# Kernel tuning notes

Hardware: AMD Instinct MI355X
Metric: run time of the kernel (lower is better)

## Reference

```python
import jax, jax.numpy as jnp
import numpy as np

DIM = 1024
HEADS = 8
DIM_HEAD = DIM // HEADS  # 128
INNER = HEADS * DIM_HEAD  # 1024
EPS = 1e-5


def _xavier(key, shape):
    fan_out, fan_in = shape
    limit = float(np.sqrt(6.0 / (fan_in + fan_out)))
    return jax.random.uniform(key, shape, jnp.float32, -limit, limit)


def setup_inputs() -> dict:
    key = jax.random.key(0)
    ks = jax.random.split(key, 5)
    bs, patch = 16, 2048
    q = jax.random.normal(ks[0], (bs, patch, DIM), jnp.float32)
    kv = jax.random.normal(ks[1], (bs, patch, DIM), jnp.float32)
    Wq = _xavier(ks[2], (INNER, DIM))          # torch Linear weight [out, in]
    Wkv = _xavier(ks[3], (2 * INNER, DIM))
    Wo = _xavier(ks[4], (DIM, INNER))
    gamma_m = jnp.ones((DIM,), jnp.float32)
    beta_m = jnp.zeros((DIM,), jnp.float32)
    gamma_l = jnp.ones((DIM,), jnp.float32)
    beta_l = jnp.zeros((DIM,), jnp.float32)
    return {"q": q, "kv": kv, "gamma_m": gamma_m, "beta_m": beta_m,
            "gamma_l": gamma_l, "beta_l": beta_l, "Wq": Wq, "Wkv": Wkv, "Wo": Wo}


def _layernorm(x, gamma, beta):
    mu = jnp.mean(x, axis=-1, keepdims=True)
    var = jnp.mean(jnp.square(x - mu), axis=-1, keepdims=True)
    return (x - mu) * jax.lax.rsqrt(var + EPS) * gamma + beta


def reference(q, kv, gamma_m, beta_m, gamma_l, beta_l, Wq, Wkv, Wo):
    bs, patch, _ = kv.shape
    scale = DIM_HEAD ** (-0.5)
    qn = _layernorm(q, gamma_m, beta_m)
    kvn = _layernorm(kv, gamma_l, beta_l)
    query = qn @ Wq.T                               # [bs, patch, inner]
    kv_proj = kvn @ Wkv.T                           # [bs, patch, 2*inner]
    key_, value = jnp.split(kv_proj, 2, axis=-1)
    query = query.reshape(bs, patch, HEADS, DIM_HEAD)
    key_ = key_.reshape(bs, patch, HEADS, DIM_HEAD)
    value = value.reshape(bs, patch, HEADS, DIM_HEAD)
    # NOTE: faithful to source: heads axis is NOT moved to batch, so
    # attention is over the HEADS dim per position: scores [bs, patch, heads, heads]
    scores = jnp.einsum('bphd,bpgd->bphg', query, key_) * scale
    weights = jax.nn.softmax(scores, axis=-1)
    context = jnp.einsum('bphg,bpgd->bphd', weights, value)
    context = context.reshape(bs, patch, INNER)
    return context @ Wo.T
```

## Files before the change

kernel.cpp:

```cpp
#include <hip/hip_runtime.h>

typedef unsigned short ushort_t;
typedef __attribute__((ext_vector_type(4))) unsigned short ushort4_t;
typedef __attribute__((ext_vector_type(8))) unsigned short ushort8;
typedef __attribute__((ext_vector_type(8))) __bf16 bf16x8;
typedef __attribute__((ext_vector_type(4))) float f32x4;

typedef const unsigned int __attribute__((address_space(1)))* gas_ptr;
typedef unsigned int __attribute__((address_space(3)))* las_ptr;

__device__ __forceinline__ float b2f(unsigned short u) {
    union { unsigned int i; float f; } x; x.i = ((unsigned int)u) << 16; return x.f;
}
__device__ __forceinline__ unsigned short f2b(float f) {
    union { float f; unsigned int i; } x; x.f = f;
    unsigned int r = (x.i + 0x7fffu + ((x.i >> 16) & 1u)) >> 16;
    return (unsigned short)r;
}

__global__ __launch_bounds__(256) void cvt_kernel(const float* __restrict__ wq,
        const float* __restrict__ wkv, const float* __restrict__ wo,
        ushort_t* __restrict__ yq, ushort_t* __restrict__ ykv, ushort_t* __restrict__ yo) {
    int b = blockIdx.x;
    const float* x; ushort_t* y; size_t off;
    if (b < 1024)      { x = wq;  y = yq;  off = (size_t)b * 1024; }
    else if (b < 3072) { x = wkv; y = ykv; off = (size_t)(b - 1024) * 1024; }
    else               { x = wo;  y = yo;  off = (size_t)(b - 3072) * 1024; }
    size_t i = off + threadIdx.x * 4;
    f32x4 v = *(const f32x4*)(x + i);
    ushort4_t o;
    #pragma unroll
    for (int t = 0; t < 4; ++t) o[t] = f2b(v[t]);
    *(ushort4_t*)(y + i) = o;
}

__global__ __launch_bounds__(256) void ln_kernel(const float* __restrict__ x,
        const float* __restrict__ gamma, const float* __restrict__ beta,
        ushort_t* __restrict__ y) {
    int wave = threadIdx.x >> 6, lane = threadIdx.x & 63;
    size_t row = (size_t)blockIdx.x * 4 + wave;
    const float* xr = x + row * 1024;
    f32x4 v[4];
    #pragma unroll
    for (int c = 0; c < 4; ++c) v[c] = *(const f32x4*)(xr + c * 256 + lane * 4);
    float s = 0.f, s2 = 0.f;
    #pragma unroll
    for (int c = 0; c < 4; ++c)
        #pragma unroll
        for (int t = 0; t < 4; ++t) { s += v[c][t]; s2 += v[c][t] * v[c][t]; }
    #pragma unroll
    for (int off = 1; off < 64; off <<= 1) {
        s  += __shfl_xor(s,  off, 64);
        s2 += __shfl_xor(s2, off, 64);
    }
    float mean = s * (1.0f / 1024.0f);
    float var  = fmaxf(s2 * (1.0f / 1024.0f) - mean * mean, 0.f);
    float rstd = rsqrtf(var + 1e-5f);
    ushort_t* yr = y + row * 1024;
    #pragma unroll
    for (int c = 0; c < 4; ++c) {
        f32x4 g = *(const f32x4*)(gamma + c * 256 + lane * 4);
        f32x4 b = *(const f32x4*)(beta  + c * 256 + lane * 4);
        ushort4_t o;
        #pragma unroll
        for (int t = 0; t < 4; ++t)
            o[t] = f2b((v[c][t] - mean) * rstd * g[t] + b[t]);
        *(ushort4_t*)(yr + c * 256 + lane * 4) = o;
    }
}


#define STG_A(BUFB, RBASE, KT) \
    __builtin_amdgcn_global_load_lds((gas_ptr)(Ap + (size_t)(RBASE) * K + (KT)), \
        (las_ptr)(lds + (BUFB) * 32768 + (RBASE) * 64 + tid * 8), 16, 0, 0)
#define STG_B(BUFB, RBASE, KT) \
    __builtin_amdgcn_global_load_lds((gas_ptr)(Bp + (size_t)(RBASE) * K + (KT)), \
        (las_ptr)(lds + (BUFB) * 32768 + 16384 + (RBASE) * 64 + tid * 8), 16, 0, 0)

#define RD_A(CB, QM) do { _Pragma("unroll") \
    for (int fm = 0; fm < 4; ++fm) { \
        a[fm][0] = *(const bf16x8*)(lds + (CB) * 32768 + aB + (QM) * 4096 + fm * 1024 + ce0); \
        a[fm][1] = *(const bf16x8*)(lds + (CB) * 32768 + aB + (QM) * 4096 + fm * 1024 + ce1); \
    } } while (0)
#define RD_B(CB, QN, BV) do { _Pragma("unroll") \
    for (int fn = 0; fn < 2; ++fn) { \
        BV[fn][0] = *(const bf16x8*)(lds + (CB) * 32768 + bB + (QN) * 2048 + fn * 1024 + ce0); \
        BV[fn][1] = *(const bf16x8*)(lds + (CB) * 32768 + bB + (QN) * 2048 + fn * 1024 + ce1); \
    } } while (0)

#define MFMA_Q(QM, QN, BV) do { _Pragma("unroll") \
    for (int fm = 0; fm < 4; ++fm) { _Pragma("unroll") \
        for (int fn = 0; fn < 2; ++fn) { \
            acc[(QM) * 4 + fm][(QN) * 2 + fn] = __builtin_amdgcn_mfma_f32_16x16x32_bf16( \
                a[fm][0], BV[fn][0], acc[(QM) * 4 + fm][(QN) * 2 + fn], 0, 0, 0); \
            acc[(QM) * 4 + fm][(QN) * 2 + fn] = __builtin_amdgcn_mfma_f32_16x16x32_bf16( \
                a[fm][1], BV[fn][1], acc[(QM) * 4 + fm][(QN) * 2 + fn], 0, 0, 0); \
    } } } while (0)

#define PH_PRE() do { __builtin_amdgcn_s_barrier(); \
    asm volatile("s_waitcnt lgkmcnt(0)" ::: "memory"); \
    __builtin_amdgcn_s_setprio(1); } while (0)
#define PH_POST() do { __builtin_amdgcn_s_setprio(0); \
    __builtin_amdgcn_s_barrier(); } while (0)

#define KTILE(CB, KTN, KTNN) do { \
     \
    STG_A((CB) ^ 1, 64, KTN); STG_A((CB) ^ 1, 192, KTN); \
    RD_A(CB, 0); RD_B(CB, 0, b0); \
    PH_PRE(); MFMA_Q(0, 0, b0); PH_POST(); \
     \
    STG_B((CB) ^ 1, 128, KTN); STG_B((CB) ^ 1, 192, KTN); \
    RD_B(CB, 1, b1); \
    PH_PRE(); MFMA_Q(0, 1, b1); PH_POST(); \
     \
    STG_A(CB, 0, KTNN); STG_A(CB, 128, KTNN); \
    RD_A(CB, 1); \
    PH_PRE(); MFMA_Q(1, 0, b0); PH_POST(); \
     \
    STG_B(CB, 0, KTNN); STG_B(CB, 64, KTNN); \
    PH_PRE(); MFMA_Q(1, 1, b1); \
    __builtin_amdgcn_s_setprio(0); \
    asm volatile("s_waitcnt vmcnt(4)" ::: "memory"); \
    __builtin_amdgcn_s_barrier(); \
} while (0)

template <bool OUT_F32>
__global__ __launch_bounds__(512) void gemm256(const ushort_t* __restrict__ A,
        const ushort_t* __restrict__ B, void* __restrict__ Cv,
        int M, int N, int K) {
    __shared__ ushort_t lds[65536];
    const int tid = threadIdx.x;
    const int lane = tid & 63;
    const int wid = tid >> 6;
    const int wr = wid >> 2, wc = wid & 3;
    const int r16 = lane & 15, q4 = lane >> 4;

    const unsigned nwgx = gridDim.x;
    const unsigned lin = blockIdx.y * nwgx + blockIdx.x;
    const unsigned chunk = (nwgx * gridDim.y) >> 3;
    const unsigned nl = (lin & 7) * chunk + (lin >> 3);
    const int m0 = (int)(nl / nwgx) * 256, n0 = (int)(nl % nwgx) * 256;
    const int NT = K >> 6;

    const int rA = tid >> 3;
    const int cS = ((tid & 7) * 8) ^ ((rA & 7) * 8);
    const ushort_t* Ap = A + (size_t)(m0 + rA) * K + cS;
    const ushort_t* Bp = B + (size_t)(n0 + rA) * K + cS;

    const int ce0 = (q4 * 8) ^ ((lane & 7) * 8);
    const int ce1 = ce0 ^ 32;
    const int aB = (wr * 128 + r16) * 64;
    const int bB = 16384 + (wc * 64 + r16) * 64;

    f32x4 acc[8][4];
    #pragma unroll
    for (int i = 0; i < 8; ++i)
        #pragma unroll
        for (int j = 0; j < 4; ++j)
            acc[i][j] = (f32x4){0.f, 0.f, 0.f, 0.f};
    bf16x8 a[4][2], b0[2][2], b1[2][2];

    STG_A(0, 0, 0); STG_A(0, 128, 0); STG_B(0, 0, 0); STG_B(0, 64, 0);
    STG_A(0, 64, 0); STG_A(0, 192, 0); STG_B(0, 128, 0); STG_B(0, 192, 0);
    STG_A(1, 0, 64); STG_A(1, 128, 64); STG_B(1, 0, 64); STG_B(1, 64, 64);
    asm volatile("s_waitcnt vmcnt(4)" ::: "memory");
    __builtin_amdgcn_s_barrier();

    for (int tt = 0; tt < (NT >> 1); ++tt) {
        const int t = tt << 1;
        const int k1 = (t + 1) << 6;
        int k2 = (t + 2) << 6; if (k2 > K - 64) k2 = K - 64;
        int k3 = (t + 3) << 6; if (k3 > K - 64) k3 = K - 64;
        KTILE(0, k1, k2);
        KTILE(1, k2, k3);
    }

    #pragma unroll
    for (int fm = 0; fm < 8; ++fm) {
        #pragma unroll
        for (int rr = 0; rr < 4; ++rr) {
            int rowC = m0 + wr * 128 + fm * 16 + q4 * 4 + rr;
            if (OUT_F32) {
                float* Cr = (float*)Cv + (size_t)rowC * N + n0 + wc * 64 + r16;
                #pragma unroll
                for (int fn = 0; fn < 4; ++fn)
                    Cr[fn * 16] = acc[fm][fn][rr];
            } else {
                ushort_t* Cr = (ushort_t*)Cv + (size_t)rowC * N + n0 + wc * 64 + r16;
                #pragma unroll
                for (int fn = 0; fn < 4; ++fn)
                    Cr[fn * 16] = f2b(acc[fm][fn][rr]);
            }
        }
    }
}

__global__ __launch_bounds__(256) void attn_kernel(const ushort_t* qin,
        const ushort_t* kvin, ushort_t* outp) {
    __shared__ ushort_t sm[4 * 3072];
    int wave = threadIdx.x >> 6, lane = threadIdx.x & 63;
    size_t p = (size_t)blockIdx.x * 4 + wave;
    ushort_t* sQ = sm + wave * 3072;
    ushort_t* sKV = sQ + 1024;
    const ushort_t* qp  = qin  + p * 1024;
    const ushort_t* kvp = kvin + p * 2048;
    *(ushort8*)(sQ + lane * 8)       = *(const ushort8*)(qp + lane * 8);
    *(ushort8*)(sQ + 512 + lane * 8) = *(const ushort8*)(qp + 512 + lane * 8);
    #pragma unroll
    for (int s = 0; s < 4; ++s)
        *(ushort8*)(sKV + s * 512 + lane * 8) = *(const ushort8*)(kvp + s * 512 + lane * 8);
    __syncthreads();
    int h = lane >> 3;
    int g = lane & 7;
    float sc = 0.f;
    #pragma unroll
    for (int j = 0; j < 128; j += 8) {
        ushort8 a = *(const ushort8*)(sQ + h * 128 + j);
        ushort8 k = *(const ushort8*)(sKV + g * 128 + j);
        #pragma unroll
        for (int t = 0; t < 8; ++t) sc += b2f(a[t]) * b2f(k[t]);
    }
    sc *= 0.08838834764831845f;
    float mx = sc;
    mx = fmaxf(mx, __shfl_xor(mx, 1, 64));
    mx = fmaxf(mx, __shfl_xor(mx, 2, 64));
    mx = fmaxf(mx, __shfl_xor(mx, 4, 64));
    float e = __expf(sc - mx);
    float den = e;
    den += __shfl_xor(den, 1, 64);
    den += __shfl_xor(den, 2, 64);
    den += __shfl_xor(den, 4, 64);
    float w = e / den;
    int d0 = (lane & 7) * 16;
    int gb = lane & 56;
    float accv[16];
    #pragma unroll
    for (int t = 0; t < 16; ++t) accv[t] = 0.f;
    #pragma unroll
    for (int gg = 0; gg < 8; ++gg) {
        float wg = __shfl(w, gb + gg, 64);
        const ushort_t* vr = sKV + 1024 + gg * 128 + d0;
        ushort8 x0 = *(const ushort8*)(vr);
        ushort8 x1 = *(const ushort8*)(vr + 8);
        #pragma unroll
        for (int t = 0; t < 8; ++t) {
            accv[t]     += wg * b2f(x0[t]);
            accv[8 + t] += wg * b2f(x1[t]);
        }
    }
    ushort8 o0, o1;
    #pragma unroll
    for (int t = 0; t < 8; ++t) { o0[t] = f2b(accv[t]); o1[t] = f2b(accv[8 + t]); }
    ushort_t* op = outp + p * 1024 + h * 128 + d0;
    *(ushort8*)(op)     = o0;
    *(ushort8*)(op + 8) = o1;
}

extern "C" void kernel_launch(void* const* d_in, const int* in_sizes, int n_in,
                              void* d_out, int out_size, void* d_ws, size_t ws_size,
                              hipStream_t stream) {
    const float* q   = (const float*)d_in[0];
    const float* kv  = (const float*)d_in[1];
    const float* gm  = (const float*)d_in[2];
    const float* bm  = (const float*)d_in[3];
    const float* gl  = (const float*)d_in[4];
    const float* bl  = (const float*)d_in[5];
    const float* Wq  = (const float*)d_in[6];
    const float* Wkv = (const float*)d_in[7];
    const float* Wo  = (const float*)d_in[8];
    float* out = (float*)d_out;

    const int ROWS = 16 * 2048;
    ushort_t* ws     = (ushort_t*)d_ws;
    ushort_t* norm   = ws;
    ushort_t* kvproj = norm + (size_t)ROWS * 1024;
    ushort_t* qbuf   = kvproj + (size_t)ROWS * 2048;
    ushort_t* wq_b   = qbuf + (size_t)ROWS * 1024;
    ushort_t* wkv_b  = wq_b + 1024 * 1024;
    ushort_t* wo_b   = wkv_b + 2048 * 1024;

    cvt_kernel<<<4096, 256, 0, stream>>>(Wq, Wkv, Wo, wq_b, wkv_b, wo_b);
    ln_kernel<<<ROWS / 4, 256, 0, stream>>>(kv, gl, bl, norm);
    gemm256<false><<<dim3(2048 / 256, ROWS / 256), 512, 0, stream>>>(norm, wkv_b, kvproj, ROWS, 2048, 1024);
    ln_kernel<<<ROWS / 4, 256, 0, stream>>>(q, gm, bm, norm);
    gemm256<false><<<dim3(1024 / 256, ROWS / 256), 512, 0, stream>>>(norm, wq_b, qbuf, ROWS, 1024, 1024);
    attn_kernel<<<ROWS / 4, 256, 0, stream>>>(qbuf, kvproj, qbuf);
    gemm256<true><<<dim3(1024 / 256, ROWS / 256), 512, 0, stream>>>(qbuf, wo_b, out, ROWS, 1024, 1024);
}
```

Measured before the change: 660.8 us.

## Make GEMMs persistent with XCD-aware tile mapping and prefetch next tile during epilogue

The three GEMM launches now use a fixed grid of 256 workgroups. Each workgroup loops over several 256x256 output tiles that share one N column, using an XCD-aware mapping of block id to M and N. The next tile's LDS prologue loads are issued before the current tile's epilogue stores, so global loads overlap the output writes and launch and tail costs shrink. The attention kernel also drops its __syncthreads, because each wave only reads LDS data it wrote itself. This relies on in-order LDS access within a wave, and the persistent schedule risks load imbalance if tiles finish unevenly.

```diff
diff --git a/kernel.cpp b/kernel.cpp
--- a/kernel.cpp
+++ b/kernel.cpp
@@ -70,12 +70,21 @@
 }
 
 
-#define STG_A(BUFB, RBASE, KT) \
-    __builtin_amdgcn_global_load_lds((gas_ptr)(Ap + (size_t)(RBASE) * K + (KT)), \
+#define STG_AP(P, BUFB, RBASE, KT) \
+    __builtin_amdgcn_global_load_lds((gas_ptr)((P) + (size_t)(RBASE) * K + (KT)), \
         (las_ptr)(lds + (BUFB) * 32768 + (RBASE) * 64 + tid * 8), 16, 0, 0)
-#define STG_B(BUFB, RBASE, KT) \
+#define STG_BP(BUFB, RBASE, KT) \
     __builtin_amdgcn_global_load_lds((gas_ptr)(Bp + (size_t)(RBASE) * K + (KT)), \
         (las_ptr)(lds + (BUFB) * 32768 + 16384 + (RBASE) * 64 + tid * 8), 16, 0, 0)
+#define STG_A(BUFB, RBASE, KT) STG_AP(Ap, BUFB, RBASE, KT)
+#define STG_B(BUFB, RBASE, KT) STG_BP(BUFB, RBASE, KT)
+
+#define PROLOGUE(P, KA) do { \
+    STG_AP(P, 0, 0, KA); STG_AP(P, 0, 128, KA); STG_BP(0, 0, KA); STG_BP(0, 64, KA); \
+    STG_AP(P, 0, 64, KA); STG_AP(P, 0, 192, KA); STG_BP(0, 128, KA); STG_BP(0, 192, KA); \
+    STG_AP(P, 1, 0, (KA) + 64); STG_AP(P, 1, 128, (KA) + 64); \
+    STG_BP(1, 0, (KA) + 64); STG_BP(1, 64, (KA) + 64); \
+} while (0)
 
 #define RD_A(CB, QM) do { _Pragma("unroll") \
     for (int fm = 0; fm < 4; ++fm) { \
@@ -135,16 +144,16 @@
     const int wr = wid >> 2, wc = wid & 3;
     const int r16 = lane & 15, q4 = lane >> 4;
 
-    const unsigned nwgx = gridDim.x;
-    const unsigned lin = blockIdx.y * nwgx + blockIdx.x;
-    const unsigned chunk = (nwgx * gridDim.y) >> 3;
-    const unsigned nl = (lin & 7) * chunk + (lin >> 3);
-    const int m0 = (int)(nl / nwgx) * 256, n0 = (int)(nl % nwgx) * 256;
+    const int bid = blockIdx.x;
+    const int xcd = bid & 7, j = bid >> 3;
+    const int nx = N >> 8;
+    const int lnx = (nx == 8) ? 3 : 2;
+    const int iters = nx >> 1;
+    const int n0 = (j & (nx - 1)) * 256;
     const int NT = K >> 6;
 
     const int rA = tid >> 3;
     const int cS = ((tid & 7) * 8) ^ ((rA & 7) * 8);
-    const ushort_t* Ap = A + (size_t)(m0 + rA) * K + cS;
     const ushort_t* Bp = B + (size_t)(n0 + rA) * K + cS;
 
     const int ce0 = (q4 * 8) ^ ((lane & 7) * 8);
@@ -153,44 +162,60 @@
     const int bB = 16384 + (wc * 64 + r16) * 64;
 
     f32x4 acc[8][4];
-    #pragma unroll
-    for (int i = 0; i < 8; ++i)
-        #pragma unroll
-        for (int j = 0; j < 4; ++j)
-            acc[i][j] = (f32x4){0.f, 0.f, 0.f, 0.f};
     bf16x8 a[4][2], b0[2][2], b1[2][2];
 
-    STG_A(0, 0, 0); STG_A(0, 128, 0); STG_B(0, 0, 0); STG_B(0, 64, 0);
-    STG_A(0, 64, 0); STG_A(0, 192, 0); STG_B(0, 128, 0); STG_B(0, 192, 0);
-    STG_A(1, 0, 64); STG_A(1, 128, 64); STG_B(1, 0, 64); STG_B(1, 64, 64);
+    int m0 = ((xcd << 4) + (j >> lnx)) << 8;
+    const int dm0 = 256 << (5 - lnx);
+    const ushort_t* Ap = A + (size_t)(m0 + rA) * K + cS;
+
+    PROLOGUE(Ap, 0);
     asm volatile("s_waitcnt vmcnt(4)" ::: "memory");
     __builtin_amdgcn_s_barrier();
 
-    for (int tt = 0; tt < (NT >> 1); ++tt) {
-        const int t = tt << 1;
-        const int k1 = (t + 1) << 6;
-        int k2 = (t + 2) << 6; if (k2 > K - 64) k2 = K - 64;
-        int k3 = (t + 3) << 6; if (k3 > K - 64) k3 = K - 64;
-        KTILE(0, k1, k2);
-        KTILE(1, k2, k3);
-    }
-
-    #pragma unroll
-    for (int fm = 0; fm < 8; ++fm) {
-        #pragma unroll
-        for (int rr = 0; rr < 4; ++rr) {
-            int rowC = m0 + wr * 128 + fm * 16 + q4 * 4 + rr;
-            if (OUT_F32) {
-                float* Cr = (float*)Cv + (size_t)rowC * N + n0 + wc * 64 + r16;
-                #pragma unroll
-                for (int fn = 0; fn < 4; ++fn)
-                    Cr[fn * 16] = acc[fm][fn][rr];
-            } else {
-                ushort_t* Cr = (ushort_t*)Cv + (size_t)rowC * N + n0 + wc * 64 + r16;
-                #pragma unroll
-                for (int fn = 0; fn < 4; ++fn)
-                    Cr[fn * 16] = f2b(acc[fm][fn][rr]);
+    for (int r = 0; r < iters; ++r) {
+        #pragma unroll
+        for (int i = 0; i < 8; ++i)
+            #pragma unroll
+            for (int jj = 0; jj < 4; ++jj)
+                acc[i][jj] = (f32x4){0.f, 0.f, 0.f, 0.f};
+
+        for (int tt = 0; tt < (NT >> 1); ++tt) {
+            const int t = tt << 1;
+            const int k1 = (t + 1) << 6;
+            int k2 = (t + 2) << 6; if (k2 > K - 64) k2 = K - 64;
+            int k3 = (t + 3) << 6; if (k3 > K - 64) k3 = K - 64;
+            KTILE(0, k1, k2);
+            KTILE(1, k2, k3);
+        }
+
+        const bool more = (r + 1 < iters);
+        asm volatile("s_waitcnt vmcnt(0)" ::: "memory");
+        const ushort_t* ApN = Ap + (size_t)dm0 * K;
+        if (more) PROLOGUE(ApN, 0);
+
+        #pragma unroll
+        for (int fm = 0; fm < 8; ++fm) {
+            #pragma unroll
+            for (int rr = 0; rr < 4; ++rr) {
+                int rowC = m0 + wr * 128 + fm * 16 + q4 * 4 + rr;
+                if (OUT_F32) {
+                    float* Cr = (float*)Cv + (size_t)rowC * N + n0 + wc * 64 + r16;
+                    #pragma unroll
+                    for (int fn = 0; fn < 4; ++fn)
+                        Cr[fn * 16] = acc[fm][fn][rr];
+                } else {
+                    ushort_t* Cr = (ushort_t*)Cv + (size_t)rowC * N + n0 + wc * 64 + r16;
+                    #pragma unroll
+                    for (int fn = 0; fn < 4; ++fn)
+                        Cr[fn * 16] = f2b(acc[fm][fn][rr]);
+                }
             }
+        }
+        if (more) {
+            m0 += dm0;
+            Ap = ApN;
+            asm volatile("s_waitcnt vmcnt(4)" ::: "memory");
+            __builtin_amdgcn_s_barrier();
         }
     }
 }
@@ -209,16 +234,15 @@
     #pragma unroll
     for (int s = 0; s < 4; ++s)
         *(ushort8*)(sKV + s * 512 + lane * 8) = *(const ushort8*)(kvp + s * 512 + lane * 8);
-    __syncthreads();
     int h = lane >> 3;
     int g = lane & 7;
     float sc = 0.f;
     #pragma unroll
-    for (int j = 0; j < 128; j += 8) {
-        ushort8 a = *(const ushort8*)(sQ + h * 128 + j);
-        ushort8 k = *(const ushort8*)(sKV + g * 128 + j);
-        #pragma unroll
-        for (int t = 0; t < 8; ++t) sc += b2f(a[t]) * b2f(k[t]);
+    for (int jv = 0; jv < 128; jv += 8) {
+        ushort8 aq = *(const ushort8*)(sQ + h * 128 + jv);
+        ushort8 kq = *(const ushort8*)(sKV + g * 128 + jv);
+        #pragma unroll
+        for (int t = 0; t < 8; ++t) sc += b2f(aq[t]) * b2f(kq[t]);
     }
     sc *= 0.08838834764831845f;
     float mx = sc;
@@ -281,9 +305,9 @@
 
     cvt_kernel<<<4096, 256, 0, stream>>>(Wq, Wkv, Wo, wq_b, wkv_b, wo_b);
     ln_kernel<<<ROWS / 4, 256, 0, stream>>>(kv, gl, bl, norm);
-    gemm256<false><<<dim3(2048 / 256, ROWS / 256), 512, 0, stream>>>(norm, wkv_b, kvproj, ROWS, 2048, 1024);
+    gemm256<false><<<256, 512, 0, stream>>>(norm, wkv_b, kvproj, ROWS, 2048, 1024);
     ln_kernel<<<ROWS / 4, 256, 0, stream>>>(q, gm, bm, norm);
-    gemm256<false><<<dim3(1024 / 256, ROWS / 256), 512, 0, stream>>>(norm, wq_b, qbuf, ROWS, 1024, 1024);
+    gemm256<false><<<256, 512, 0, stream>>>(norm, wq_b, qbuf, ROWS, 1024, 1024);
     attn_kernel<<<ROWS / 4, 256, 0, stream>>>(qbuf, kvproj, qbuf);
-    gemm256<true><<<dim3(1024 / 256, ROWS / 256), 512, 0, stream>>>(qbuf, wo_b, out, ROWS, 1024, 1024);
-}
+    gemm256<true><<<256, 512, 0, stream>>>(qbuf, wo_b, out, ROWS, 1024, 1024);
+}
```

New measurement: 635.5 us. 1.04x faster.
